# Kernel tuning notes

Hardware: AMD Instinct MI355X
Metric: run time of the kernel (lower is better)

Reference implementation:

```python
import jax, jax.numpy as jnp
import numpy as np

INPUT_SIZE = 512
HIDDEN_SIZE = 1024
SEQ_LEN = 512
BATCH = 64

def _xavier(key, shape):
    fan_out, fan_in = shape
    bound = float(np.sqrt(6.0 / (fan_in + fan_out)))
    return jax.random.uniform(key, shape, jnp.float32, -bound, bound)

def setup_inputs() -> dict:
    key = jax.random.key(0)
    ks = jax.random.split(key, 5)
    return {
        "x_seq": jax.random.normal(ks[0], (SEQ_LEN, BATCH, INPUT_SIZE), jnp.float32),
        "h0": jax.random.normal(ks[1], (BATCH, HIDDEN_SIZE), jnp.float32),
        "U_c": _xavier(ks[2], (HIDDEN_SIZE, INPUT_SIZE)),
        "w_c": jnp.ones((HIDDEN_SIZE,), jnp.float32),
        "b_c": jnp.zeros((HIDDEN_SIZE,), jnp.float32),
        "U_a": _xavier(ks[3], (HIDDEN_SIZE, INPUT_SIZE)),
        "w_a": jnp.ones((HIDDEN_SIZE,), jnp.float32),
        "b_a": jnp.zeros((HIDDEN_SIZE,), jnp.float32),
        "U_h": _xavier(ks[4], (HIDDEN_SIZE, INPUT_SIZE)),
        "b_h": jnp.zeros((HIDDEN_SIZE,), jnp.float32),
    }

def reference(x_seq, h0, U_c, w_c, b_c, U_a, w_a, b_a, U_h, b_h):
    # Batch the three input projections across all timesteps (the compute-heavy
    # GEMMs), then run the inherently-sequential gated recurrence with lax.scan.
    xc = jnp.einsum('tbi,hi->tbh', x_seq, U_c) + b_c  # [T, B, H]
    xa = jnp.einsum('tbi,hi->tbh', x_seq, U_a) + b_a
    xh = jnp.einsum('tbi,hi->tbh', x_seq, U_h) + b_h

    def step(h, proj):
        pc, pa, ph = proj
        c = jax.nn.sigmoid(pc + w_c * h)
        a = 1.0 + jnp.tanh(pa + w_a * h)
        h_new = c * h + (1.0 - c) * jnp.tanh(ph + a * h)
        return h_new, h_new

    h_last, y_seq = jax.lax.scan(step, h0, (xc, xa, xh))
    return (y_seq, (h_last,))
```

## Files before the change

### kernel.cpp

```cpp
#include <hip/hip_runtime.h>
#include <cstdint>
#include <cstddef>

#define T_SEQ 512
#define BATCH 64
#define IN_SZ 512
#define HID   1024
#define BH    (BATCH*HID)
#define M_TOT (T_SEQ*BATCH)
#define D_CH  16

typedef float f32x4 __attribute__((ext_vector_type(4)));
typedef _Float16 f16x8 __attribute__((ext_vector_type(8)));

__device__ inline unsigned short f2h(float f){
  union { _Float16 h; unsigned short u; } v;
  v.h = (_Float16)f;
  return v.u;
}
__device__ inline float h2f(unsigned short s){
  union { unsigned short u; _Float16 h; } v; v.u = s;
  return (float)v.h;
}

__device__ inline float sigm_f(float x){ return 1.f/(1.f + __expf(-x)); }
__device__ inline float tanh_f(float x){ float e = __expf(2.f*x); return 1.f - 2.f/(e + 1.f); }

__device__ inline void async16(const void* g, void* l){
  __builtin_amdgcn_global_load_lds(
      (__attribute__((address_space(1))) void*)g,
      (__attribute__((address_space(3))) void*)l,
      16, 0, 0);
}

#define XBLK 16384
__global__ __launch_bounds__(256) void cvt_all(
    const float* __restrict__ x,  const float* __restrict__ Uc,
    const float* __restrict__ Ua, const float* __restrict__ Uh,
    unsigned short* __restrict__ xb, unsigned short* __restrict__ U0,
    unsigned short* __restrict__ U1, unsigned short* __restrict__ U2)
{
  int b = blockIdx.x;
  const float* in; unsigned short* out; int i;
  if (b < XBLK){
    in = x; out = xb; i = b*256 + threadIdx.x;
  } else {
    int r = b - XBLK;
    int which = r >> 9;
    int lb = r & 511;
    i = lb*256 + threadIdx.x;
    in  = (which==0) ? Uc : (which==1) ? Ua : Uh;
    out = (which==0) ? U0 : (which==1) ? U1 : U2;
  }
  float4 v = ((const float4*)in)[i];
  ushort4 o;
  o.x = f2h(v.x); o.y = f2h(v.y); o.z = f2h(v.z); o.w = f2h(v.w);
  ((ushort4*)out)[i] = o;
}

__global__ __launch_bounds__(512, 2) void gemm3(
    const unsigned short* __restrict__ xb,
    const unsigned short* __restrict__ U0,
    const unsigned short* __restrict__ U1,
    const unsigned short* __restrict__ U2,
    const float* __restrict__ b0, const float* __restrict__ b1, const float* __restrict__ b2,
    unsigned short* out0, unsigned short* out1, void* out2, int ph_f16)
{
  __shared__ __align__(16) unsigned char smem_raw[131072];

  const int tid  = threadIdx.x;
  const int wave = tid >> 6, lane = tid & 63;
  const int quad = lane >> 4, l16 = lane & 15;

  const int bid  = blockIdx.x;
  const int xcd  = bid & 7;
  const int slot = bid >> 3;
  const int mbl  = slot / 12;
  const int inner= slot - mbl*12;
  const int mb   = xcd*16 + mbl;
  const int z    = inner % 3;
  const int nb   = inner / 3;

  const int m0 = mb * 256, n0 = nb * 256;
  const unsigned short* Um = (z==0) ? U0 : (z==1) ? U1 : U2;
  const float* bias        = (z==0) ? b0 : (z==1) ? b1 : b2;
  const int wm = wave >> 2, wn = wave & 3;

  const int laneRow = lane >> 2;
  const int cg8     = ((lane & 3) ^ ((lane >> 3) & 3)) << 3;
  const unsigned short* srcA = xb + (size_t)m0 * IN_SZ;
  const unsigned short* srcB = Um + (size_t)n0 * IN_SZ;

  const int cxa = l16*64 + ((quad ^ ((l16 >> 1) & 3)) << 4);

  auto stageA = [&](int tile, int kh){
    unsigned char* dst = smem_raw + (((tile & 1)*2 + kh) << 14);
#pragma unroll
    for (int j = 0; j < 2; ++j){
      const unsigned short* g = srcA + (size_t)((wave*2 + j)*16 + laneRow)*IN_SZ
                                + tile*64 + kh*32 + cg8;
      async16(g, dst + (wave*2 + j)*1024);
    }
  };
  auto stageB = [&](int tile, int kh){
    unsigned char* dst = smem_raw + 65536 + (((tile & 1)*2 + kh) << 14);
#pragma unroll
    for (int j = 0; j < 2; ++j){
      const unsigned short* g = srcB + (size_t)((wave*2 + j)*16 + laneRow)*IN_SZ
                                + tile*64 + kh*32 + cg8;
      async16(g, dst + (wave*2 + j)*1024);
    }
  };

  const f32x4 zf = {0.f, 0.f, 0.f, 0.f};
  f32x4 acc[8][4];
#pragma unroll
  for (int i = 0; i < 8; ++i)
#pragma unroll
    for (int j = 0; j < 4; ++j) acc[i][j] = zf;

  stageA(0,0); stageB(0,0); stageA(0,1); stageB(0,1);
  stageA(1,0); stageB(1,0); stageA(1,1);
  asm volatile("s_waitcnt vmcnt(10)" ::: "memory");
  __builtin_amdgcn_s_barrier();

#define CLUSTER(B0_, B1_, N0_, N1_)                                                      \
  __builtin_amdgcn_s_barrier();                                                          \
  asm volatile("s_waitcnt lgkmcnt(0)" ::: "memory");                                     \
  __builtin_amdgcn_s_setprio(1);                                                         \
  _Pragma("unroll")                                                                      \
  for (int im_ = 0; im_ < 8; ++im_){                                                     \
    acc[im_][N0_] = __builtin_amdgcn_mfma_f32_16x16x32_f16(a0[im_], B0_, acc[im_][N0_], 0,0,0); \
    acc[im_][N1_] = __builtin_amdgcn_mfma_f32_16x16x32_f16(a0[im_], B1_, acc[im_][N1_], 0,0,0); \
  }                                                                                      \
  __builtin_amdgcn_s_setprio(0);                                                         \
  __builtin_amdgcn_s_barrier();

  f16x8 a0[8];
#pragma unroll
  for (int g = 0; g < 8; ++g){
    const int buf = g & 1;
    const unsigned char* Ab0 = smem_raw + ((buf*2 + 0) << 14);
    const unsigned char* Ab1 = smem_raw + ((buf*2 + 1) << 14);
    const unsigned char* Bb0 = smem_raw + 65536 + ((buf*2 + 0) << 14);
    const unsigned char* Bb1 = smem_raw + 65536 + ((buf*2 + 1) << 14);

#pragma unroll
    for (int im = 0; im < 8; ++im)
      a0[im] = *(const f16x8*)(Ab0 + wm*8192 + im*1024 + cxa);
    f16x8 q0 = *(const f16x8*)(Bb0 + wn*4096 + 0*1024 + cxa);
    f16x8 q1 = *(const f16x8*)(Bb0 + wn*4096 + 1*1024 + cxa);
    if (g < 7) stageB(g+1, 1);
    CLUSTER(q0, q1, 0, 1)

    f16x8 q2 = *(const f16x8*)(Bb0 + wn*4096 + 2*1024 + cxa);
    f16x8 q3 = *(const f16x8*)(Bb0 + wn*4096 + 3*1024 + cxa);
    if (g < 6) stageA(g+2, 0);
    if (g < 6)      { asm volatile("s_waitcnt vmcnt(10)" ::: "memory"); }
    else if (g == 6){ asm volatile("s_waitcnt vmcnt(8)"  ::: "memory"); }
    else            { asm volatile("s_waitcnt vmcnt(0)"  ::: "memory"); }
    CLUSTER(q2, q3, 2, 3)

#pragma unroll
    for (int im = 0; im < 8; ++im)
      a0[im] = *(const f16x8*)(Ab1 + wm*8192 + im*1024 + cxa);
    q0 = *(const f16x8*)(Bb1 + wn*4096 + 0*1024 + cxa);
    q1 = *(const f16x8*)(Bb1 + wn*4096 + 1*1024 + cxa);
    if (g < 6) stageB(g+2, 0);
    CLUSTER(q0, q1, 0, 1)

    q2 = *(const f16x8*)(Bb1 + wn*4096 + 2*1024 + cxa);
    q3 = *(const f16x8*)(Bb1 + wn*4096 + 3*1024 + cxa);
    if (g < 6) stageA(g+2, 1);
    if (g < 6)      { asm volatile("s_waitcnt vmcnt(10)" ::: "memory"); }
    else if (g == 6){ asm volatile("s_waitcnt vmcnt(4)"  ::: "memory"); }
    CLUSTER(q2, q3, 2, 3)
  }
#undef CLUSTER

  float bv[4];
#pragma unroll
  for (int in = 0; in < 4; ++in) bv[in] = bias[n0 + wn*64 + in*16 + l16];

  if (z == 2 && !ph_f16) {
    float* o32 = (float*)out2;
#pragma unroll
    for (int im = 0; im < 8; ++im)
#pragma unroll
      for (int r = 0; r < 4; ++r){
        int grow = m0 + wm*128 + im*16 + quad*4 + r;
        size_t rb = (size_t)grow * HID;
#pragma unroll
        for (int in = 0; in < 4; ++in)
          o32[rb + n0 + wn*64 + in*16 + l16] = acc[im][in][r] + bv[in];
      }
    return;
  }

  unsigned short* op = (z==0) ? out0 : (z==1) ? out1 : (unsigned short*)out2;
  unsigned short* sw = (unsigned short*)smem_raw + wave*4608;
#pragma unroll
  for (int h = 0; h < 2; ++h){
#pragma unroll
    for (int i4 = 0; i4 < 4; ++i4){
      int im = h*4 + i4;
#pragma unroll
      for (int r = 0; r < 4; ++r){
        int lr = i4*16 + quad*4 + r;
#pragma unroll
        for (int in = 0; in < 4; ++in)
          sw[lr*72 + in*16 + l16] = f2h(acc[im][in][r] + bv[in]);
      }
    }
    asm volatile("s_waitcnt lgkmcnt(0)" ::: "memory");
#pragma unroll
    for (int i = 0; i < 8; ++i){
      int lr = i*8 + (lane >> 3);
      int ch = lane & 7;
      uint4 v = *(const uint4*)(sw + lr*72 + ch*8);
      int grow = m0 + wm*128 + h*64 + lr;
      *(uint4*)(op + (size_t)grow*HID + n0 + wn*64 + ch*8) = v;
    }
    if (h == 0) asm volatile("s_waitcnt lgkmcnt(0)" ::: "memory");
  }
}

template <bool PH16>
__global__ __launch_bounds__(256) void scan_k(
    const unsigned short* __restrict__ pc, const unsigned short* __restrict__ pa,
    const void* __restrict__ phv,
    float* __restrict__ y,
    const float* __restrict__ h0, const float* __restrict__ wc, const float* __restrict__ wa,
    float* __restrict__ hlast)
{
  __shared__ __align__(16) unsigned char sm[65536];
  const int tid  = threadIdx.x;
  const int wave = tid >> 6, lane = tid & 63;
  const int col0 = blockIdx.x * 256;
  const int idx  = col0 + tid;
  const int hidx = idx & (HID - 1);

  float h = h0[idx];
  const float wcv = wc[hidx], wav = wa[hidx];
  const unsigned short* ph16 = (const unsigned short*)phv;
  const float*          ph32 = (const float*)phv;

  unsigned char* pcL = sm;
  unsigned char* paL = sm + 16384;
  unsigned char* phL = sm + 32768;

  auto stage = [&](int c){
    const int b  = c & 1;
    const int t0 = c * D_CH;
#pragma unroll
    for (int j = 0; j < 2; ++j){
      const int tr  = wave*2 + j*8;
      const int row = tr + (lane >> 5);
      const int ce  = (lane & 31) * 8;
      async16(pc + (size_t)(t0+row)*BH + col0 + ce, pcL + b*8192 + tr*512);
      async16(pa + (size_t)(t0+row)*BH + col0 + ce, paL + b*8192 + tr*512);
    }
    if (PH16){
#pragma unroll
      for (int j = 0; j < 2; ++j){
        const int tr  = wave*2 + j*8;
        const int row = tr + (lane >> 5);
        const int ce  = (lane & 31) * 8;
        async16(ph16 + (size_t)(t0+row)*BH + col0 + ce, phL + b*8192 + tr*512);
      }
    } else {
#pragma unroll
      for (int j = 0; j < 4; ++j){
        const int t = wave + j*4;
        async16(ph32 + (size_t)(t0+t)*BH + col0 + lane*4, phL + b*16384 + t*1024);
      }
    }
  };

  stage(0);
  asm volatile("s_waitcnt vmcnt(0)" ::: "memory");
  __builtin_amdgcn_s_barrier();
  __builtin_amdgcn_sched_barrier(0);

  constexpr int NC = T_SEQ / D_CH;
  for (int c = 0; c < NC; ++c){
    if (c + 1 < NC) stage(c + 1);
    const int b  = c & 1;
    const int t0 = c * D_CH;
    const unsigned short* pcb   = (const unsigned short*)(pcL + b*8192)  + tid;
    const unsigned short* pab   = (const unsigned short*)(paL + b*8192)  + tid;
    const unsigned short* phb16 = (const unsigned short*)(phL + b*8192)  + tid;
    const float*          phb32 = (const float*)(phL + b*16384) + tid;
#pragma unroll
    for (int i = 0; i < D_CH; ++i){
      float pcv = h2f(pcb[i*256]);
      float pav = h2f(pab[i*256]);
      float ph_ = PH16 ? h2f(phb16[i*256]) : phb32[i*256];
      float cc = sigm_f(pcv + wcv*h);
      float a  = 1.f + tanh_f(pav + wav*h);
      float hc = tanh_f(ph_ + a*h);
      h = cc*h + (1.f - cc)*hc;
      y[(size_t)(t0 + i)*BH + idx] = h;
    }
    if (c + 1 < NC){
      asm volatile("s_waitcnt vmcnt(16)" ::: "memory");
      __builtin_amdgcn_s_barrier();
      __builtin_amdgcn_sched_barrier(0);
    }
  }
  hlast[idx] = h;
}

extern "C" void kernel_launch(void* const* d_in, const int* in_sizes, int n_in,
                              void* d_out, int out_size, void* d_ws, size_t ws_size,
                              hipStream_t stream)
{
  const float* x  = (const float*)d_in[0];
  const float* h0 = (const float*)d_in[1];
  const float* Uc = (const float*)d_in[2];
  const float* wc = (const float*)d_in[3];
  const float* bc = (const float*)d_in[4];
  const float* Ua = (const float*)d_in[5];
  const float* wa = (const float*)d_in[6];
  const float* ba = (const float*)d_in[7];
  const float* Uh = (const float*)d_in[8];
  const float* bh = (const float*)d_in[9];

  float* y     = (float*)d_out;
  float* hlast = y + (size_t)T_SEQ * BH;

  const size_t szP16 = (size_t)T_SEQ * BH * 2;
  const size_t szX16 = (size_t)M_TOT * IN_SZ * 2;
  const size_t szU16 = (size_t)HID * IN_SZ * 2;

  const size_t base = 2*szP16 + szX16 + 3*szU16;
  const bool ph_sep = ws_size >= base + szP16;

  char* w = (char*)d_ws;
  unsigned short* pc16 = (unsigned short*)w;
  unsigned short* pa16 = (unsigned short*)(w + szP16);
  unsigned short* xb   = (unsigned short*)(w + 2*szP16);
  unsigned short* U0b  = (unsigned short*)(w + 2*szP16 + szX16);
  unsigned short* U1b  = U0b + szU16/2;
  unsigned short* U2b  = U1b + szU16/2;
  unsigned short* ph16 = (unsigned short*)(w + base);

  cvt_all<<<XBLK + 3*512, 256, 0, stream>>>(x, Uc, Ua, Uh, xb, U0b, U1b, U2b);

  void* phbuf = ph_sep ? (void*)ph16 : (void*)y;
  gemm3<<<1536, 512, 0, stream>>>(xb, U0b, U1b, U2b, bc, ba, bh,
                                  pc16, pa16, phbuf, ph_sep ? 1 : 0);

  if (ph_sep)
    scan_k<true><<<BH/256, 256, 0, stream>>>(pc16, pa16, (const void*)ph16,
                                             y, h0, wc, wa, hlast);
  else
    scan_k<false><<<BH/256, 256, 0, stream>>>(pc16, pa16, (const void*)y,
                                              y, h0, wc, wa, hlast);
}
```

Baseline: 372.2 us.

## Fuse three projection GEMMs per block, move bias into scan, triple-buffer scan

The GEMM kernel now runs 512 blocks. Each block loops over all three weight matrices for the same A tile, so the x tile rows are reloaded from L2/LDS-staged pipelines instead of being handled by three separate blocks. The K-loop pipeline is restructured into a simpler per-half-tile double buffer that prefetches across the z boundary. Each z result is dumped through a dedicated LDS area before the accumulators are reset. Bias addition moves from the GEMM epilogue into the scan kernel, and the scan kernel goes from double to triple buffering of staged projections. The trade-offs are larger LDS use (about 146KB limits GEMM occupancy), fewer blocks, which may underfill the GPU, and a longer serial dependency per block.

```diff
diff --git a/kernel.cpp b/kernel.cpp
--- a/kernel.cpp
+++ b/kernel.cpp
@@ -63,10 +63,9 @@
     const unsigned short* __restrict__ U0,
     const unsigned short* __restrict__ U1,
     const unsigned short* __restrict__ U2,
-    const float* __restrict__ b0, const float* __restrict__ b1, const float* __restrict__ b2,
     unsigned short* out0, unsigned short* out1, void* out2, int ph_f16)
 {
-  __shared__ __align__(16) unsigned char smem_raw[131072];
+  __shared__ __align__(16) unsigned char smem_raw[149504];
 
   const int tid  = threadIdx.x;
   const int wave = tid >> 6, lane = tid & 63;
@@ -75,41 +74,33 @@
   const int bid  = blockIdx.x;
   const int xcd  = bid & 7;
   const int slot = bid >> 3;
-  const int mbl  = slot / 12;
-  const int inner= slot - mbl*12;
+  const int mbl  = slot >> 2;
+  const int nb   = slot & 3;
   const int mb   = xcd*16 + mbl;
-  const int z    = inner % 3;
-  const int nb   = inner / 3;
-
   const int m0 = mb * 256, n0 = nb * 256;
-  const unsigned short* Um = (z==0) ? U0 : (z==1) ? U1 : U2;
-  const float* bias        = (z==0) ? b0 : (z==1) ? b1 : b2;
   const int wm = wave >> 2, wn = wave & 3;
 
   const int laneRow = lane >> 2;
   const int cg8     = ((lane & 3) ^ ((lane >> 3) & 3)) << 3;
   const unsigned short* srcA = xb + (size_t)m0 * IN_SZ;
-  const unsigned short* srcB = Um + (size_t)n0 * IN_SZ;
-
   const int cxa = l16*64 + ((quad ^ ((l16 >> 1) & 3)) << 4);
 
-  auto stageA = [&](int tile, int kh){
-    unsigned char* dst = smem_raw + (((tile & 1)*2 + kh) << 14);
-#pragma unroll
-    for (int j = 0; j < 2; ++j){
-      const unsigned short* g = srcA + (size_t)((wave*2 + j)*16 + laneRow)*IN_SZ
-                                + tile*64 + kh*32 + cg8;
-      async16(g, dst + (wave*2 + j)*1024);
-    }
-  };
-  auto stageB = [&](int tile, int kh){
-    unsigned char* dst = smem_raw + 65536 + (((tile & 1)*2 + kh) << 14);
-#pragma unroll
-    for (int j = 0; j < 2; ++j){
-      const unsigned short* g = srcB + (size_t)((wave*2 + j)*16 + laneRow)*IN_SZ
-                                + tile*64 + kh*32 + cg8;
-      async16(g, dst + (wave*2 + j)*1024);
-    }
+  auto stA = [&](int par, int kk, int kh){
+    unsigned char* dst = smem_raw + ((par*2 + kh) << 14);
+#pragma unroll
+    for (int j = 0; j < 2; ++j)
+      async16(srcA + (size_t)((wave*2 + j)*16 + laneRow)*IN_SZ + kk + kh*32 + cg8,
+              dst + (wave*2 + j)*1024);
+  };
+  auto stB = [&](const unsigned short* sB, int par, int kk, int kh){
+    unsigned char* dst = smem_raw + 65536 + ((par*2 + kh) << 14);
+#pragma unroll
+    for (int j = 0; j < 2; ++j)
+      async16(sB + (size_t)((wave*2 + j)*16 + laneRow)*IN_SZ + kk + kh*32 + cg8,
+              dst + (wave*2 + j)*1024);
+  };
+  auto usel = [&](int zz)->const unsigned short*{
+    return ((zz==0) ? U0 : (zz==1) ? U1 : U2) + (size_t)n0 * IN_SZ;
   };
 
   const f32x4 zf = {0.f, 0.f, 0.f, 0.f};
@@ -119,110 +110,128 @@
 #pragma unroll
     for (int j = 0; j < 4; ++j) acc[i][j] = zf;
 
-  stageA(0,0); stageB(0,0); stageA(0,1); stageB(0,1);
-  stageA(1,0); stageB(1,0); stageA(1,1);
-  asm volatile("s_waitcnt vmcnt(10)" ::: "memory");
+  auto dump_z = [&](int zc){
+    if (zc == 2 && !ph_f16){
+      float* o32 = (float*)out2;
+#pragma unroll
+      for (int im = 0; im < 8; ++im)
+#pragma unroll
+        for (int r = 0; r < 4; ++r){
+          int grow = m0 + wm*128 + im*16 + quad*4 + r;
+          size_t rb = (size_t)grow * HID;
+#pragma unroll
+          for (int in = 0; in < 4; ++in)
+            o32[rb + n0 + wn*64 + in*16 + l16] = acc[im][in][r];
+        }
+      return;
+    }
+    unsigned short* op = (zc==0) ? out0 : (zc==1) ? out1 : (unsigned short*)out2;
+    unsigned short* sw = (unsigned short*)(smem_raw + 131072) + wave*1152;
+#pragma unroll
+    for (int im = 0; im < 8; ++im){
+#pragma unroll
+      for (int r = 0; r < 4; ++r){
+        int lr = quad*4 + r;
+#pragma unroll
+        for (int in = 0; in < 4; ++in)
+          sw[lr*72 + in*16 + l16] = f2h(acc[im][in][r]);
+      }
+      asm volatile("s_waitcnt lgkmcnt(0)" ::: "memory");
+#pragma unroll
+      for (int i = 0; i < 2; ++i){
+        int lr = i*8 + (lane >> 3);
+        int ch = lane & 7;
+        uint4 v = *(const uint4*)(sw + lr*72 + ch*8);
+        int grow = m0 + wm*128 + im*16 + lr;
+        *(uint4*)(op + (size_t)grow*HID + n0 + wn*64 + ch*8) = v;
+      }
+      asm volatile("s_waitcnt lgkmcnt(0)" ::: "memory");
+    }
+  };
+
+  {
+    const unsigned short* B0s = usel(0);
+    stA(0, 0, 0); stB(B0s, 0, 0, 0); stA(0, 0, 1); stB(B0s, 0, 0, 1);
+  }
+  asm volatile("s_waitcnt vmcnt(4)" ::: "memory");
   __builtin_amdgcn_s_barrier();
 
-#define CLUSTER(B0_, B1_, N0_, N1_)                                                      \
-  __builtin_amdgcn_s_barrier();                                                          \
-  asm volatile("s_waitcnt lgkmcnt(0)" ::: "memory");                                     \
-  __builtin_amdgcn_s_setprio(1);                                                         \
-  _Pragma("unroll")                                                                      \
-  for (int im_ = 0; im_ < 8; ++im_){                                                     \
-    acc[im_][N0_] = __builtin_amdgcn_mfma_f32_16x16x32_f16(a0[im_], B0_, acc[im_][N0_], 0,0,0); \
-    acc[im_][N1_] = __builtin_amdgcn_mfma_f32_16x16x32_f16(a0[im_], B1_, acc[im_][N1_], 0,0,0); \
-  }                                                                                      \
-  __builtin_amdgcn_s_setprio(0);                                                         \
-  __builtin_amdgcn_s_barrier();
-
-  f16x8 a0[8];
-#pragma unroll
-  for (int g = 0; g < 8; ++g){
-    const int buf = g & 1;
-    const unsigned char* Ab0 = smem_raw + ((buf*2 + 0) << 14);
-    const unsigned char* Ab1 = smem_raw + ((buf*2 + 1) << 14);
-    const unsigned char* Bb0 = smem_raw + 65536 + ((buf*2 + 0) << 14);
-    const unsigned char* Bb1 = smem_raw + 65536 + ((buf*2 + 1) << 14);
-
-#pragma unroll
-    for (int im = 0; im < 8; ++im)
-      a0[im] = *(const f16x8*)(Ab0 + wm*8192 + im*1024 + cxa);
-    f16x8 q0 = *(const f16x8*)(Bb0 + wn*4096 + 0*1024 + cxa);
-    f16x8 q1 = *(const f16x8*)(Bb0 + wn*4096 + 1*1024 + cxa);
-    if (g < 7) stageB(g+1, 1);
-    CLUSTER(q0, q1, 0, 1)
-
-    f16x8 q2 = *(const f16x8*)(Bb0 + wn*4096 + 2*1024 + cxa);
-    f16x8 q3 = *(const f16x8*)(Bb0 + wn*4096 + 3*1024 + cxa);
-    if (g < 6) stageA(g+2, 0);
-    if (g < 6)      { asm volatile("s_waitcnt vmcnt(10)" ::: "memory"); }
-    else if (g == 6){ asm volatile("s_waitcnt vmcnt(8)"  ::: "memory"); }
-    else            { asm volatile("s_waitcnt vmcnt(0)"  ::: "memory"); }
-    CLUSTER(q2, q3, 2, 3)
-
-#pragma unroll
-    for (int im = 0; im < 8; ++im)
-      a0[im] = *(const f16x8*)(Ab1 + wm*8192 + im*1024 + cxa);
-    q0 = *(const f16x8*)(Bb1 + wn*4096 + 0*1024 + cxa);
-    q1 = *(const f16x8*)(Bb1 + wn*4096 + 1*1024 + cxa);
-    if (g < 6) stageB(g+2, 0);
-    CLUSTER(q0, q1, 0, 1)
-
-    q2 = *(const f16x8*)(Bb1 + wn*4096 + 2*1024 + cxa);
-    q3 = *(const f16x8*)(Bb1 + wn*4096 + 3*1024 + cxa);
-    if (g < 6) stageA(g+2, 1);
-    if (g < 6)      { asm volatile("s_waitcnt vmcnt(10)" ::: "memory"); }
-    else if (g == 6){ asm volatile("s_waitcnt vmcnt(4)"  ::: "memory"); }
-    CLUSTER(q2, q3, 2, 3)
+#define MFMA16(AARR, BQ, NCOL)                                                            \
+  _Pragma("unroll")                                                                       \
+  for (int im_ = 0; im_ < 8; ++im_)                                                       \
+    acc[im_][NCOL] = __builtin_amdgcn_mfma_f32_16x16x32_f16(AARR[im_], BQ, acc[im_][NCOL], 0,0,0);
+
+  for (int z = 0; z < 3; ++z){
+    const unsigned short* Uc_ = usel(z);
+    const unsigned short* Un_ = usel(z < 2 ? z + 1 : 2);
+#pragma unroll
+    for (int g = 0; g < 8; ++g){
+      const int par   = g & 1;
+      const int npar  = par ^ 1;
+      const int knext = ((g + 1) & 7) * 64;
+      const bool haveNext = (z < 2) || (g < 7);
+      const unsigned short* Bn = (g == 7) ? Un_ : Uc_;
+      const unsigned char* As0 = smem_raw + ((par*2 + 0) << 14);
+      const unsigned char* As1 = smem_raw + ((par*2 + 1) << 14);
+      const unsigned char* Bs0 = smem_raw + 65536 + ((par*2 + 0) << 14);
+      const unsigned char* Bs1 = smem_raw + 65536 + ((par*2 + 1) << 14);
+
+      if (haveNext){ stA(npar, knext, 0); stB(Bn, npar, knext, 0); }
+      {
+        f16x8 aC[8], q0, q1, q2, q3;
+#pragma unroll
+        for (int im = 0; im < 8; ++im)
+          aC[im] = *(const f16x8*)(As0 + wm*8192 + im*1024 + cxa);
+        q0 = *(const f16x8*)(Bs0 + wn*4096 + 0*1024 + cxa);
+        q1 = *(const f16x8*)(Bs0 + wn*4096 + 1*1024 + cxa);
+        __builtin_amdgcn_s_setprio(1);
+        MFMA16(aC, q0, 0)
+        MFMA16(aC, q1, 1)
+        q2 = *(const f16x8*)(Bs0 + wn*4096 + 2*1024 + cxa);
+        q3 = *(const f16x8*)(Bs0 + wn*4096 + 3*1024 + cxa);
+        MFMA16(aC, q2, 2)
+        MFMA16(aC, q3, 3)
+        __builtin_amdgcn_s_setprio(0);
+      }
+      if (z == 2 && g == 7)      { asm volatile("s_waitcnt vmcnt(0)"  ::: "memory"); }
+      else if (g == 0 && z > 0)  { asm volatile("s_waitcnt vmcnt(20)" ::: "memory"); }
+      else                       { asm volatile("s_waitcnt vmcnt(4)"  ::: "memory"); }
+      __builtin_amdgcn_s_barrier();
+
+      if (haveNext){ stA(npar, knext, 1); stB(Bn, npar, knext, 1); }
+      {
+        f16x8 aC[8], q0, q1, q2, q3;
+#pragma unroll
+        for (int im = 0; im < 8; ++im)
+          aC[im] = *(const f16x8*)(As1 + wm*8192 + im*1024 + cxa);
+        q0 = *(const f16x8*)(Bs1 + wn*4096 + 0*1024 + cxa);
+        q1 = *(const f16x8*)(Bs1 + wn*4096 + 1*1024 + cxa);
+        __builtin_amdgcn_s_setprio(1);
+        MFMA16(aC, q0, 0)
+        MFMA16(aC, q1, 1)
+        q2 = *(const f16x8*)(Bs1 + wn*4096 + 2*1024 + cxa);
+        q3 = *(const f16x8*)(Bs1 + wn*4096 + 3*1024 + cxa);
+        MFMA16(aC, q2, 2)
+        MFMA16(aC, q3, 3)
+        __builtin_amdgcn_s_setprio(0);
+      }
+      if (!(z == 2 && g == 7)){
+        asm volatile("s_waitcnt vmcnt(4)" ::: "memory");
+        __builtin_amdgcn_s_barrier();
+      }
+
+      if (g == 7){
+        dump_z(z);
+        if (z < 2){
+#pragma unroll
+          for (int i = 0; i < 8; ++i)
+#pragma unroll
+            for (int j = 0; j < 4; ++j) acc[i][j] = zf;
+        }
+      }
+    }
   }
-#undef CLUSTER
-
-  float bv[4];
-#pragma unroll
-  for (int in = 0; in < 4; ++in) bv[in] = bias[n0 + wn*64 + in*16 + l16];
-
-  if (z == 2 && !ph_f16) {
-    float* o32 = (float*)out2;
-#pragma unroll
-    for (int im = 0; im < 8; ++im)
-#pragma unroll
-      for (int r = 0; r < 4; ++r){
-        int grow = m0 + wm*128 + im*16 + quad*4 + r;
-        size_t rb = (size_t)grow * HID;
-#pragma unroll
-        for (int in = 0; in < 4; ++in)
-          o32[rb + n0 + wn*64 + in*16 + l16] = acc[im][in][r] + bv[in];
-      }
-    return;
-  }
-
-  unsigned short* op = (z==0) ? out0 : (z==1) ? out1 : (unsigned short*)out2;
-  unsigned short* sw = (unsigned short*)smem_raw + wave*4608;
-#pragma unroll
-  for (int h = 0; h < 2; ++h){
-#pragma unroll
-    for (int i4 = 0; i4 < 4; ++i4){
-      int im = h*4 + i4;
-#pragma unroll
-      for (int r = 0; r < 4; ++r){
-        int lr = i4*16 + quad*4 + r;
-#pragma unroll
-        for (int in = 0; in < 4; ++in)
-          sw[lr*72 + in*16 + l16] = f2h(acc[im][in][r] + bv[in]);
-      }
-    }
-    asm volatile("s_waitcnt lgkmcnt(0)" ::: "memory");
-#pragma unroll
-    for (int i = 0; i < 8; ++i){
-      int lr = i*8 + (lane >> 3);
-      int ch = lane & 7;
-      uint4 v = *(const uint4*)(sw + lr*72 + ch*8);
-      int grow = m0 + wm*128 + h*64 + lr;
-      *(uint4*)(op + (size_t)grow*HID + n0 + wn*64 + ch*8) = v;
-    }
-    if (h == 0) asm volatile("s_waitcnt lgkmcnt(0)" ::: "memory");
-  }
+#undef MFMA16
 }
 
 template <bool PH16>
@@ -231,9 +240,10 @@
     const void* __restrict__ phv,
     float* __restrict__ y,
     const float* __restrict__ h0, const float* __restrict__ wc, const float* __restrict__ wa,
+    const float* __restrict__ bc, const float* __restrict__ ba, const float* __restrict__ bh,
     float* __restrict__ hlast)
 {
-  __shared__ __align__(16) unsigned char sm[65536];
+  __shared__ __align__(16) unsigned char sm[98304];
   const int tid  = threadIdx.x;
   const int wave = tid >> 6, lane = tid & 63;
   const int col0 = blockIdx.x * 256;
@@ -242,15 +252,15 @@
 
   float h = h0[idx];
   const float wcv = wc[hidx], wav = wa[hidx];
+  const float bcv = bc[hidx], bav = ba[hidx], bhv = bh[hidx];
   const unsigned short* ph16 = (const unsigned short*)phv;
   const float*          ph32 = (const float*)phv;
 
   unsigned char* pcL = sm;
-  unsigned char* paL = sm + 16384;
-  unsigned char* phL = sm + 32768;
-
-  auto stage = [&](int c){
-    const int b  = c & 1;
+  unsigned char* paL = sm + 24576;
+  unsigned char* phL = sm + 49152;
+
+  auto stage = [&](int c, int b){
     const int t0 = c * D_CH;
 #pragma unroll
     for (int j = 0; j < 2; ++j){
@@ -277,36 +287,44 @@
     }
   };
 
-  stage(0);
-  asm volatile("s_waitcnt vmcnt(0)" ::: "memory");
+  stage(0, 0); stage(1, 1);
+  if (PH16) asm volatile("s_waitcnt vmcnt(6)" ::: "memory");
+  else      asm volatile("s_waitcnt vmcnt(8)" ::: "memory");
   __builtin_amdgcn_s_barrier();
   __builtin_amdgcn_sched_barrier(0);
 
   constexpr int NC = T_SEQ / D_CH;
+  int bcur = 0, b2 = 2;
   for (int c = 0; c < NC; ++c){
-    if (c + 1 < NC) stage(c + 1);
-    const int b  = c & 1;
+    if (c + 2 < NC) stage(c + 2, b2);
     const int t0 = c * D_CH;
-    const unsigned short* pcb   = (const unsigned short*)(pcL + b*8192)  + tid;
-    const unsigned short* pab   = (const unsigned short*)(paL + b*8192)  + tid;
-    const unsigned short* phb16 = (const unsigned short*)(phL + b*8192)  + tid;
-    const float*          phb32 = (const float*)(phL + b*16384) + tid;
+    const unsigned short* pcb   = (const unsigned short*)(pcL + bcur*8192)  + tid;
+    const unsigned short* pab   = (const unsigned short*)(paL + bcur*8192)  + tid;
+    const unsigned short* phb16 = (const unsigned short*)(phL + bcur*8192)  + tid;
+    const float*          phb32 = (const float*)(phL + bcur*16384) + tid;
 #pragma unroll
     for (int i = 0; i < D_CH; ++i){
       float pcv = h2f(pcb[i*256]);
       float pav = h2f(pab[i*256]);
       float ph_ = PH16 ? h2f(phb16[i*256]) : phb32[i*256];
-      float cc = sigm_f(pcv + wcv*h);
-      float a  = 1.f + tanh_f(pav + wav*h);
-      float hc = tanh_f(ph_ + a*h);
+      float cc = sigm_f(pcv + bcv + wcv*h);
+      float a  = 1.f + tanh_f(pav + bav + wav*h);
+      float hc = tanh_f(ph_ + bhv + a*h);
       h = cc*h + (1.f - cc)*hc;
       y[(size_t)(t0 + i)*BH + idx] = h;
     }
     if (c + 1 < NC){
-      asm volatile("s_waitcnt vmcnt(16)" ::: "memory");
+      if (c + 2 < NC){
+        if (PH16) asm volatile("s_waitcnt vmcnt(22)" ::: "memory");
+        else      asm volatile("s_waitcnt vmcnt(24)" ::: "memory");
+      } else {
+        asm volatile("s_waitcnt vmcnt(16)" ::: "memory");
+      }
       __builtin_amdgcn_s_barrier();
       __builtin_amdgcn_sched_barrier(0);
     }
+    bcur = (bcur == 2) ? 0 : bcur + 1;
+    b2   = (b2   == 2) ? 0 : b2   + 1;
   }
   hlast[idx] = h;
 }
@@ -348,13 +366,13 @@
   cvt_all<<<XBLK + 3*512, 256, 0, stream>>>(x, Uc, Ua, Uh, xb, U0b, U1b, U2b);
 
   void* phbuf = ph_sep ? (void*)ph16 : (void*)y;
-  gemm3<<<1536, 512, 0, stream>>>(xb, U0b, U1b, U2b, bc, ba, bh,
-                                  pc16, pa16, phbuf, ph_sep ? 1 : 0);
+  gemm3<<<512, 512, 0, stream>>>(xb, U0b, U1b, U2b,
+                                 pc16, pa16, phbuf, ph_sep ? 1 : 0);
 
   if (ph_sep)
     scan_k<true><<<BH/256, 256, 0, stream>>>(pc16, pa16, (const void*)ph16,
-                                             y, h0, wc, wa, hlast);
+                                             y, h0, wc, wa, bc, ba, bh, hlast);
   else
     scan_k<false><<<BH/256, 256, 0, stream>>>(pc16, pa16, (const void*)y,
-                                              y, h0, wc, wa, hlast);
-}
+                                              y, h0, wc, wa, bc, ba, bh, hlast);
+}
```

New measurement: 446.0 us. +19.8%, slower.

## Fuse fp32-to-fp16 conversion of x into GEMM A-tile staging

Applied to the files above, without the earlier changes.

Removes the separate conversion pass over x_seq and has the projection GEMM load fp32 x directly into registers, convert to fp16, and write LDS, replacing async global-to-LDS loads for A. This eliminates a full read/write pass of the input tensor in a separate kernel. In exchange the GEMM reads twice as many bytes for A, uses more registers for in-flight A tiles, and A staging now goes through VGPRs with extra waitcnt synchronization.

```diff
diff --git a/kernel.cpp b/kernel.cpp
--- a/kernel.cpp
+++ b/kernel.cpp
@@ -33,25 +33,17 @@
       16, 0, 0);
 }
 
-#define XBLK 16384
 __global__ __launch_bounds__(256) void cvt_all(
-    const float* __restrict__ x,  const float* __restrict__ Uc,
-    const float* __restrict__ Ua, const float* __restrict__ Uh,
-    unsigned short* __restrict__ xb, unsigned short* __restrict__ U0,
-    unsigned short* __restrict__ U1, unsigned short* __restrict__ U2)
+    const float* __restrict__ Uc, const float* __restrict__ Ua, const float* __restrict__ Uh,
+    unsigned short* __restrict__ U0, unsigned short* __restrict__ U1,
+    unsigned short* __restrict__ U2)
 {
   int b = blockIdx.x;
-  const float* in; unsigned short* out; int i;
-  if (b < XBLK){
-    in = x; out = xb; i = b*256 + threadIdx.x;
-  } else {
-    int r = b - XBLK;
-    int which = r >> 9;
-    int lb = r & 511;
-    i = lb*256 + threadIdx.x;
-    in  = (which==0) ? Uc : (which==1) ? Ua : Uh;
-    out = (which==0) ? U0 : (which==1) ? U1 : U2;
-  }
+  int which = b >> 9;
+  int lb = b & 511;
+  int i = lb*256 + threadIdx.x;
+  const float* in  = (which==0) ? Uc : (which==1) ? Ua : Uh;
+  unsigned short* out = (which==0) ? U0 : (which==1) ? U1 : U2;
   float4 v = ((const float4*)in)[i];
   ushort4 o;
   o.x = f2h(v.x); o.y = f2h(v.y); o.z = f2h(v.z); o.w = f2h(v.w);
@@ -59,7 +51,7 @@
 }
 
 __global__ __launch_bounds__(512, 2) void gemm3(
-    const unsigned short* __restrict__ xb,
+    const float* __restrict__ xf,
     const unsigned short* __restrict__ U0,
     const unsigned short* __restrict__ U1,
     const unsigned short* __restrict__ U2,
@@ -88,18 +80,29 @@
 
   const int laneRow = lane >> 2;
   const int cg8     = ((lane & 3) ^ ((lane >> 3) & 3)) << 3;
-  const unsigned short* srcA = xb + (size_t)m0 * IN_SZ;
   const unsigned short* srcB = Um + (size_t)n0 * IN_SZ;
 
   const int cxa = l16*64 + ((quad ^ ((l16 >> 1) & 3)) << 4);
 
-  auto stageA = [&](int tile, int kh){
+  auto issueA = [&](int tile, int kh, float4* ar){
+#pragma unroll
+    for (int j = 0; j < 2; ++j){
+      const int row = (wave*2 + j)*16 + laneRow;
+      const float* g = xf + (size_t)(m0 + row)*IN_SZ + tile*64 + kh*32 + cg8;
+      ar[2*j]   = *(const float4*)(g);
+      ar[2*j+1] = *(const float4*)(g + 4);
+    }
+  };
+  auto writeA = [&](int tile, int kh, const float4* ar){
     unsigned char* dst = smem_raw + (((tile & 1)*2 + kh) << 14);
 #pragma unroll
     for (int j = 0; j < 2; ++j){
-      const unsigned short* g = srcA + (size_t)((wave*2 + j)*16 + laneRow)*IN_SZ
-                                + tile*64 + kh*32 + cg8;
-      async16(g, dst + (wave*2 + j)*1024);
+      f16x8 v;
+      v[0] = (_Float16)ar[2*j].x;   v[1] = (_Float16)ar[2*j].y;
+      v[2] = (_Float16)ar[2*j].z;   v[3] = (_Float16)ar[2*j].w;
+      v[4] = (_Float16)ar[2*j+1].x; v[5] = (_Float16)ar[2*j+1].y;
+      v[6] = (_Float16)ar[2*j+1].z; v[7] = (_Float16)ar[2*j+1].w;
+      *(f16x8*)(dst + (wave*2 + j)*1024 + lane*16) = v;
     }
   };
   auto stageB = [&](int tile, int kh){
@@ -119,10 +122,21 @@
 #pragma unroll
     for (int j = 0; j < 4; ++j) acc[i][j] = zf;
 
-  stageA(0,0); stageB(0,0); stageA(0,1); stageB(0,1);
-  stageA(1,0); stageB(1,0); stageA(1,1);
-  asm volatile("s_waitcnt vmcnt(10)" ::: "memory");
-  __builtin_amdgcn_s_barrier();
+  float4 ar0[4], ar1[4];
+  {
+    float4 aP0[4], aP1[4];
+    issueA(0,0,aP0); issueA(0,1,aP1);
+    asm volatile("s_waitcnt vmcnt(0)" ::: "memory");
+    writeA(0,0,aP0); writeA(0,1,aP1);
+    issueA(1,0,aP0); issueA(1,1,aP1);
+    stageB(0,0); stageB(0,1); stageB(1,0);
+    issueA(2,0,ar0);
+    asm volatile("s_waitcnt vmcnt(0)" ::: "memory");
+    writeA(1,0,aP0); writeA(1,1,aP1);
+    asm volatile("s_waitcnt lgkmcnt(0)" ::: "memory");
+    __builtin_amdgcn_sched_barrier(0);
+    __builtin_amdgcn_s_barrier();
+  }
 
 #define CLUSTER(B0_, B1_, N0_, N1_)                                                      \
   __builtin_amdgcn_s_barrier();                                                          \
@@ -150,15 +164,18 @@
       a0[im] = *(const f16x8*)(Ab0 + wm*8192 + im*1024 + cxa);
     f16x8 q0 = *(const f16x8*)(Bb0 + wn*4096 + 0*1024 + cxa);
     f16x8 q1 = *(const f16x8*)(Bb0 + wn*4096 + 1*1024 + cxa);
+    if (g < 6) issueA(g+2, 1, ar1);
     if (g < 7) stageB(g+1, 1);
     CLUSTER(q0, q1, 0, 1)
 
     f16x8 q2 = *(const f16x8*)(Bb0 + wn*4096 + 2*1024 + cxa);
     f16x8 q3 = *(const f16x8*)(Bb0 + wn*4096 + 3*1024 + cxa);
-    if (g < 6) stageA(g+2, 0);
-    if (g < 6)      { asm volatile("s_waitcnt vmcnt(10)" ::: "memory"); }
-    else if (g == 6){ asm volatile("s_waitcnt vmcnt(8)"  ::: "memory"); }
-    else            { asm volatile("s_waitcnt vmcnt(0)"  ::: "memory"); }
+    if (g < 6)      { asm volatile("s_waitcnt vmcnt(6)" ::: "memory"); }
+    else if (g == 6){ asm volatile("s_waitcnt vmcnt(4)" ::: "memory"); }
+    else            { asm volatile("s_waitcnt vmcnt(0)" ::: "memory"); }
+    if (g < 6) writeA(g+2, 0, ar0);
+    asm volatile("s_waitcnt lgkmcnt(0)" ::: "memory");
+    __builtin_amdgcn_sched_barrier(0);
     CLUSTER(q2, q3, 2, 3)
 
 #pragma unroll
@@ -166,14 +183,18 @@
       a0[im] = *(const f16x8*)(Ab1 + wm*8192 + im*1024 + cxa);
     q0 = *(const f16x8*)(Bb1 + wn*4096 + 0*1024 + cxa);
     q1 = *(const f16x8*)(Bb1 + wn*4096 + 1*1024 + cxa);
+    if (g < 5) issueA(g+3, 0, ar0);
     if (g < 6) stageB(g+2, 0);
     CLUSTER(q0, q1, 0, 1)
 
     q2 = *(const f16x8*)(Bb1 + wn*4096 + 2*1024 + cxa);
     q3 = *(const f16x8*)(Bb1 + wn*4096 + 3*1024 + cxa);
-    if (g < 6) stageA(g+2, 1);
-    if (g < 6)      { asm volatile("s_waitcnt vmcnt(10)" ::: "memory"); }
-    else if (g == 6){ asm volatile("s_waitcnt vmcnt(4)"  ::: "memory"); }
+    if (g < 5)      { asm volatile("s_waitcnt vmcnt(6)" ::: "memory"); }
+    else if (g == 5){ asm volatile("s_waitcnt vmcnt(2)" ::: "memory"); }
+    else if (g == 6){ asm volatile("s_waitcnt vmcnt(2)" ::: "memory"); }
+    if (g < 6) writeA(g+2, 1, ar1);
+    asm volatile("s_waitcnt lgkmcnt(0)" ::: "memory");
+    __builtin_amdgcn_sched_barrier(0);
     CLUSTER(q2, q3, 2, 3)
   }
 #undef CLUSTER
@@ -339,16 +360,15 @@
   char* w = (char*)d_ws;
   unsigned short* pc16 = (unsigned short*)w;
   unsigned short* pa16 = (unsigned short*)(w + szP16);
-  unsigned short* xb   = (unsigned short*)(w + 2*szP16);
   unsigned short* U0b  = (unsigned short*)(w + 2*szP16 + szX16);
   unsigned short* U1b  = U0b + szU16/2;
   unsigned short* U2b  = U1b + szU16/2;
   unsigned short* ph16 = (unsigned short*)(w + base);
 
-  cvt_all<<<XBLK + 3*512, 256, 0, stream>>>(x, Uc, Ua, Uh, xb, U0b, U1b, U2b);
+  cvt_all<<<1536, 256, 0, stream>>>(Uc, Ua, Uh, U0b, U1b, U2b);
 
   void* phbuf = ph_sep ? (void*)ph16 : (void*)y;
-  gemm3<<<1536, 512, 0, stream>>>(xb, U0b, U1b, U2b, bc, ba, bh,
+  gemm3<<<1536, 512, 0, stream>>>(x, U0b, U1b, U2b, bc, ba, bh,
                                   pc16, pa16, phbuf, ph_sep ? 1 : 0);
 
   if (ph_sep)
```

New measurement: 461.2 us. 1.24x slower.
